# Kernel tuning notes

Hardware: AMD Instinct MI355X
Metric: run time of the kernel (lower is better)

## Reference

```python
import jax, jax.numpy as jnp
import numpy as np

N, D_IN, D_ATTN = 8192, 48, 8


def setup_inputs() -> dict:
    key = jax.random.key(0)
    ks = jax.random.split(key, 9)
    s = 1.0 / np.sqrt(D_IN)
    return {
        "x": jax.random.normal(ks[0], (N, D_IN), jnp.float32),
        "Kw": jax.random.normal(ks[1], (D_IN, D_ATTN), jnp.float32) * s,
        "Kb": jax.random.normal(ks[2], (D_ATTN,), jnp.float32) * s,
        "Qw": jax.random.normal(ks[3], (D_IN, D_ATTN), jnp.float32) * s,
        "Qb": jax.random.normal(ks[4], (D_ATTN,), jnp.float32) * s,
        "Vw": jax.random.normal(ks[5], (D_IN, D_ATTN), jnp.float32) * s,
        "Vb": jax.random.normal(ks[6], (D_ATTN,), jnp.float32) * s,
        "Zw": jax.random.normal(ks[7], (D_ATTN, D_IN), jnp.float32) * (1.0 / np.sqrt(D_ATTN)),
        "Zb": jax.random.normal(ks[8], (D_IN,), jnp.float32) * (1.0 / np.sqrt(D_ATTN)),
    }


def reference(x, Kw, Kb, Qw, Qb, Vw, Vb, Zw, Zb):
    # Tiny QKV projections: [N,48] -> [N,8]
    Xk = x @ Kw + Kb
    Xq = x @ Qw + Qb
    Xv = x @ Vw + Vb
    # Attention over the batch/row dimension: [N,8]@[8,N] -> [N,N]
    scale = jnp.sqrt(jnp.asarray(D_ATTN, jnp.float32))
    AM = jax.nn.softmax(Xk @ Xq.T / scale, axis=1)  # torch F.softmax 2D default dim=1
    Z = AM @ Xv                                      # [N,8]
    return x + (Z @ Zw + Zb)                         # residual + output proj [N,48]
```

## Files before the change

### kernel.cpp

```cpp
#include <hip/hip_runtime.h>


#define PART_OFF 98560

typedef _Float16 f16x2 __attribute__((ext_vector_type(2)));

union HU { unsigned u; f16x2 h; };

static __device__ __forceinline__ unsigned pku(float a, float b) {
    auto v = __builtin_amdgcn_cvt_pkrtz(a, b);
    union { decltype(v) v2; unsigned u; } t;
    t.v2 = v;
    return t.u;
}
static __device__ __forceinline__ f16x2 asH2(unsigned u) {
    HU t; t.u = u; return t.h;
}
static __device__ __forceinline__ float fdot2(f16x2 a, f16x2 b, float c) {
#if __has_builtin(__builtin_amdgcn_fdot2)
    return __builtin_amdgcn_fdot2(a, b, c, false);
#else
    return fmaf((float)a.x, (float)b.x, fmaf((float)a.y, (float)b.y, c));
#endif
}

__global__ __launch_bounds__(256) void proj_kernel(
    const float* __restrict__ x,
    const float* __restrict__ Kw, const float* __restrict__ Kb,
    const float* __restrict__ Qw, const float* __restrict__ Qb,
    const float* __restrict__ Vw, const float* __restrict__ Vb,
    unsigned* __restrict__ Xksf16, unsigned* __restrict__ Qf16,
    unsigned* __restrict__ Vf16, unsigned int* __restrict__ qmax2_bits)
{
    __shared__ float xs[32 * 49];
    __shared__ float wAll[3 * 388];
    __shared__ float bs[24];
    __shared__ float outv[32][25];
    const int tid = threadIdx.x;
    const int r0 = blockIdx.x * 32;

    for (int i = tid; i < 1536; i += 256) {
        int r = i / 48, c = i - r * 48;
        xs[r * 49 + c] = x[r0 * 48 + i];
    }
    for (int i = tid; i < 384; i += 256) {
        wAll[i]       = Kw[i];
        wAll[388 + i] = Qw[i];
        wAll[776 + i] = Vw[i];
    }
    if (tid < 8)       bs[tid] = Kb[tid];
    else if (tid < 16) bs[tid] = Qb[tid - 8];
    else if (tid < 24) bs[tid] = Vb[tid - 16];
    __syncthreads();

    const int rl = tid >> 3;
    const int g  = tid & 7;
    const int c0 = 3 * g;
    const float* xr = &xs[rl * 49];
    const float* w0 = &wAll[((c0 + 0) >> 3) * 388 + ((c0 + 0) & 7)];
    const float* w1 = &wAll[((c0 + 1) >> 3) * 388 + ((c0 + 1) & 7)];
    const float* w2 = &wAll[((c0 + 2) >> 3) * 388 + ((c0 + 2) & 7)];
    float a0 = bs[c0], a1 = bs[c0 + 1], a2 = bs[c0 + 2];
    #pragma unroll
    for (int k = 0; k < 48; k++) {
        const float xv = xr[k];
        a0 = fmaf(xv, w0[k * 8], a0);
        a1 = fmaf(xv, w1[k * 8], a1);
        a2 = fmaf(xv, w2[k * 8], a2);
    }
    outv[rl][c0] = a0; outv[rl][c0 + 1] = a1; outv[rl][c0 + 2] = a2;
    __syncthreads();

    const float kscale = 0.51008732149f;
    if (tid < 32) {
        uint4 o;
        o.x = pku(outv[tid][0] * kscale, outv[tid][1] * kscale);
        o.y = pku(outv[tid][2] * kscale, outv[tid][3] * kscale);
        o.z = pku(outv[tid][4] * kscale, outv[tid][5] * kscale);
        o.w = pku(outv[tid][6] * kscale, outv[tid][7] * kscale);
        ((uint4*)Xksf16)[r0 + tid] = o;
    } else if (tid < 64) {
        const int r = tid - 32;
        uint4 o;
        o.x = pku(outv[r][8],  outv[r][9]);
        o.y = pku(outv[r][10], outv[r][11]);
        o.z = pku(outv[r][12], outv[r][13]);
        o.w = pku(outv[r][14], outv[r][15]);
        ((uint4*)Qf16)[r0 + r] = o;
    } else if (tid < 192) {
        const int t2 = tid - 64;
        const int p = t2 >> 3, c = t2 & 7;
        Vf16[(blockIdx.x * 16 + p) * 8 + c] =
            pku(outv[2 * p][16 + c], outv[2 * p + 1][16 + c]);
    } else if (tid < 224) {
        const int r = tid - 192;
        float n2 = 0.f;
        #pragma unroll
        for (int c = 0; c < 8; c++) n2 = fmaf(outv[r][8 + c], outv[r][8 + c], n2);
        #pragma unroll
        for (int off = 16; off > 0; off >>= 1)
            n2 = fmaxf(n2, __shfl_xor(n2, off, 64));
        if (r == 0) atomicMax(qmax2_bits, __float_as_uint(n2));
    }
}

__global__ __launch_bounds__(256) void attn_kernel(
    const unsigned* __restrict__ Xksf16, const unsigned* __restrict__ Qf16,
    const unsigned* __restrict__ Vf16,
    const unsigned int* __restrict__ qmax2_bits,
    float* __restrict__ part)
{
    const int tid   = threadIdx.x;
    const int wave  = tid >> 6, lane = tid & 63;
    const int rg    = blockIdx.x & 255;
    const int chunk = blockIdx.x >> 8;
    const int rw0   = rg * 32 + wave * 8;

    const float qmax2 = __uint_as_float(*qmax2_bits);

    f16x2 k2[8][4];
    float sinit[8], l[8], acc[8][8];
    #pragma unroll
    for (int r = 0; r < 8; r++) {
        const uint4 kv = ((const uint4*)Xksf16)[rw0 + r];
        k2[r][0] = asH2(kv.x); k2[r][1] = asH2(kv.y);
        k2[r][2] = asH2(kv.z); k2[r][3] = asH2(kv.w);
        float kn2 = fdot2(k2[r][0], k2[r][0], 0.f);
        kn2 = fdot2(k2[r][1], k2[r][1], kn2);
        kn2 = fdot2(k2[r][2], k2[r][2], kn2);
        kn2 = fdot2(k2[r][3], k2[r][3], kn2);
        sinit[r] = -sqrtf(kn2 * qmax2);
        l[r] = 0.f;
        #pragma unroll
        for (int c = 0; c < 8; c++) acc[r][c] = 0.f;
    }

    const f16x2 one2 = asH2(pku(1.f, 1.f));
    const uint4* Q4 = (const uint4*)Qf16;
    const uint4* V4 = (const uint4*)Vf16;

    const int P0 = chunk * 512 + lane;
    #pragma unroll 2
    for (int s = 0; s < 8; s++) {
        const int p = P0 + s * 64;
        const uint4 qa = Q4[2 * p];
        const uint4 qb = Q4[2 * p + 1];
        const uint4 va = V4[2 * p];
        const uint4 vb = V4[2 * p + 1];
        f16x2 qa2[4] = {asH2(qa.x), asH2(qa.y), asH2(qa.z), asH2(qa.w)};
        f16x2 qb2[4] = {asH2(qb.x), asH2(qb.y), asH2(qb.z), asH2(qb.w)};
        f16x2 v2[8]  = {asH2(va.x), asH2(va.y), asH2(va.z), asH2(va.w),
                        asH2(vb.x), asH2(vb.y), asH2(vb.z), asH2(vb.w)};
        #pragma unroll
        for (int r = 0; r < 8; r++) {
            float s0 = fdot2(k2[r][0], qa2[0], sinit[r]);
            s0 = fdot2(k2[r][1], qa2[1], s0);
            s0 = fdot2(k2[r][2], qa2[2], s0);
            s0 = fdot2(k2[r][3], qa2[3], s0);
            float s1 = fdot2(k2[r][0], qb2[0], sinit[r]);
            s1 = fdot2(k2[r][1], qb2[1], s1);
            s1 = fdot2(k2[r][2], qb2[2], s1);
            s1 = fdot2(k2[r][3], qb2[3], s1);
            const f16x2 ph = asH2(pku(__builtin_amdgcn_exp2f(s0),
                                      __builtin_amdgcn_exp2f(s1)));
            l[r] = fdot2(ph, one2, l[r]);
            acc[r][0] = fdot2(ph, v2[0], acc[r][0]);
            acc[r][1] = fdot2(ph, v2[1], acc[r][1]);
            acc[r][2] = fdot2(ph, v2[2], acc[r][2]);
            acc[r][3] = fdot2(ph, v2[3], acc[r][3]);
            acc[r][4] = fdot2(ph, v2[4], acc[r][4]);
            acc[r][5] = fdot2(ph, v2[5], acc[r][5]);
            acc[r][6] = fdot2(ph, v2[6], acc[r][6]);
            acc[r][7] = fdot2(ph, v2[7], acc[r][7]);
        }
    }

    #pragma unroll
    for (int m = 1; m < 64; m <<= 1) {
        #pragma unroll
        for (int r = 0; r < 8; r++) {
            l[r] += __shfl_xor(l[r], m, 64);
            #pragma unroll
            for (int c = 0; c < 8; c++) acc[r][c] += __shfl_xor(acc[r][c], m, 64);
        }
    }
    if (lane == 0) {
        float* pr = part + ((size_t)chunk * 8192 + rw0) * 12;
        #pragma unroll
        for (int r = 0; r < 8; r++) {
            #pragma unroll
            for (int c = 0; c < 8; c++) pr[r * 12 + c] = acc[r][c];
            pr[r * 12 + 8] = l[r];
        }
    }
}

__global__ __launch_bounds__(256) void finish_kernel(
    const float* __restrict__ x,
    const float* __restrict__ Zw, const float* __restrict__ Zb,
    const float* __restrict__ part, float* __restrict__ out)
{
    __shared__ float Zs[128 * 9];
    __shared__ float zw_s[384];
    __shared__ float zb_s[48];
    const int tid = threadIdx.x;
    const int r0 = blockIdx.x * 128;

    for (int i = tid; i < 384; i += 256) zw_s[i] = Zw[i];
    if (tid < 48) zb_s[tid] = Zb[tid];

    if (tid < 128) {
        const int row = r0 + tid;
        float a[9];
        #pragma unroll
        for (int c = 0; c < 9; c++) a[c] = 0.f;
        #pragma unroll
        for (int ch = 0; ch < 8; ch++) {
            const float* p = part + ((size_t)ch * 8192 + row) * 12;
            #pragma unroll
            for (int c = 0; c < 9; c++) a[c] += p[c];
        }
        const float inv = 1.0f / a[8];
        #pragma unroll
        for (int c = 0; c < 8; c++) Zs[tid * 9 + c] = a[c] * inv;
    }
    __syncthreads();

    for (int e = tid; e < 128 * 48; e += 256) {
        const int r = e / 48, c = e - r * 48;
        float o = x[r0 * 48 + e] + zb_s[c];
        #pragma unroll
        for (int k = 0; k < 8; k++) o = fmaf(Zs[r * 9 + k], zw_s[k * 48 + c], o);
        out[r0 * 48 + e] = o;
    }
}

extern "C" void kernel_launch(void* const* d_in, const int* in_sizes, int n_in,
                              void* d_out, int out_size, void* d_ws, size_t ws_size,
                              hipStream_t stream) {
    const float* x  = (const float*)d_in[0];
    const float* Kw = (const float*)d_in[1];
    const float* Kb = (const float*)d_in[2];
    const float* Qw = (const float*)d_in[3];
    const float* Qb = (const float*)d_in[4];
    const float* Vw = (const float*)d_in[5];
    const float* Vb = (const float*)d_in[6];
    const float* Zw = (const float*)d_in[7];
    const float* Zb = (const float*)d_in[8];
    float* out = (float*)d_out;

    float* ws = (float*)d_ws;
    unsigned* Xksf16 = (unsigned*)ws;
    unsigned* Qf16   = (unsigned*)(ws + 32768);
    unsigned* Vf16   = (unsigned*)(ws + 65536);
    unsigned int* qmax2_bits = (unsigned int*)(ws + 98304);
    float* part = ws + PART_OFF;

    (void)hipMemsetAsync(qmax2_bits, 0, sizeof(unsigned int), stream);
    proj_kernel<<<256, 256, 0, stream>>>(x, Kw, Kb, Qw, Qb, Vw, Vb,
                                         Xksf16, Qf16, Vf16, qmax2_bits);
    attn_kernel<<<2048, 256, 0, stream>>>(Xksf16, Qf16, Vf16, qmax2_bits, part);
    finish_kernel<<<64, 256, 0, stream>>>(x, Zw, Zb, part, out);
}
```

Before: 131.6 us.

## Map one query row per lane and accumulate key chunks via atomics

The attention kernel now gives each lane its own row, so the 64-step cross-lane shuffle reduction goes away. All lanes walk the same 128-key chunk, so the Q/V loads are wave-uniform broadcasts, and Q and V are interleaved into one buffer. Partial sums from the 64 chunks are combined with float atomicAdd into a zeroed accumulator, which replaces the partials buffer and the finish-kernel reduction. In exchange it adds a memset, 9 atomics per row per chunk (64-way contention per address) and nondeterministic summation order.

```diff
diff --git a/kernel.cpp b/kernel.cpp
--- a/kernel.cpp
+++ b/kernel.cpp
@@ -1,7 +1,9 @@
 #include <hip/hip_runtime.h>
 
 
-#define PART_OFF 98560
+#define QV_OFF   32768
+#define QMAX_OFF 98304
+#define ACC_OFF  98560
 
 typedef _Float16 f16x2 __attribute__((ext_vector_type(2)));
 
@@ -29,8 +31,8 @@
     const float* __restrict__ Kw, const float* __restrict__ Kb,
     const float* __restrict__ Qw, const float* __restrict__ Qb,
     const float* __restrict__ Vw, const float* __restrict__ Vb,
-    unsigned* __restrict__ Xksf16, unsigned* __restrict__ Qf16,
-    unsigned* __restrict__ Vf16, unsigned int* __restrict__ qmax2_bits)
+    unsigned* __restrict__ Xksf16, unsigned* __restrict__ QV,
+    unsigned int* __restrict__ qmax2_bits)
 {
     __shared__ float xs[32 * 49];
     __shared__ float wAll[3 * 388];
@@ -81,17 +83,18 @@
         ((uint4*)Xksf16)[r0 + tid] = o;
     } else if (tid < 64) {
         const int r = tid - 32;
+        const int j = r0 + r;
         uint4 o;
         o.x = pku(outv[r][8],  outv[r][9]);
         o.y = pku(outv[r][10], outv[r][11]);
         o.z = pku(outv[r][12], outv[r][13]);
         o.w = pku(outv[r][14], outv[r][15]);
-        ((uint4*)Qf16)[r0 + r] = o;
+        ((uint4*)QV)[(j >> 1) * 4 + (j & 1)] = o;
     } else if (tid < 192) {
         const int t2 = tid - 64;
         const int p = t2 >> 3, c = t2 & 7;
-        Vf16[(blockIdx.x * 16 + p) * 8 + c] =
-            pku(outv[2 * p][16 + c], outv[2 * p + 1][16 + c]);
+        const int pg = blockIdx.x * 16 + p;
+        QV[pg * 16 + 8 + c] = pku(outv[2 * p][16 + c], outv[2 * p + 1][16 + c]);
     } else if (tid < 224) {
         const int r = tid - 192;
         float n2 = 0.f;
@@ -105,100 +108,70 @@
 }
 
 __global__ __launch_bounds__(256) void attn_kernel(
-    const unsigned* __restrict__ Xksf16, const unsigned* __restrict__ Qf16,
-    const unsigned* __restrict__ Vf16,
+    const unsigned* __restrict__ Xksf16, const unsigned* __restrict__ QV,
     const unsigned int* __restrict__ qmax2_bits,
-    float* __restrict__ part)
+    float* __restrict__ accG)
 {
     const int tid   = threadIdx.x;
     const int wave  = tid >> 6, lane = tid & 63;
-    const int rg    = blockIdx.x & 255;
-    const int chunk = blockIdx.x >> 8;
-    const int rw0   = rg * 32 + wave * 8;
+    const int rgrp  = blockIdx.x & 31;
+    const int chunk = blockIdx.x >> 5;
+    const int row   = rgrp * 256 + wave * 64 + lane;
 
     const float qmax2 = __uint_as_float(*qmax2_bits);
 
-    f16x2 k2[8][4];
-    float sinit[8], l[8], acc[8][8];
+    const uint4 kv = ((const uint4*)Xksf16)[row];
+    f16x2 k2[4] = {asH2(kv.x), asH2(kv.y), asH2(kv.z), asH2(kv.w)};
+    float kn2 = fdot2(k2[0], k2[0], 0.f);
+    kn2 = fdot2(k2[1], k2[1], kn2);
+    kn2 = fdot2(k2[2], k2[2], kn2);
+    kn2 = fdot2(k2[3], k2[3], kn2);
+    const float sinit = -sqrtf(kn2 * qmax2);
+
+    float l = 0.f, acc[8];
     #pragma unroll
-    for (int r = 0; r < 8; r++) {
-        const uint4 kv = ((const uint4*)Xksf16)[rw0 + r];
-        k2[r][0] = asH2(kv.x); k2[r][1] = asH2(kv.y);
-        k2[r][2] = asH2(kv.z); k2[r][3] = asH2(kv.w);
-        float kn2 = fdot2(k2[r][0], k2[r][0], 0.f);
-        kn2 = fdot2(k2[r][1], k2[r][1], kn2);
-        kn2 = fdot2(k2[r][2], k2[r][2], kn2);
-        kn2 = fdot2(k2[r][3], k2[r][3], kn2);
-        sinit[r] = -sqrtf(kn2 * qmax2);
-        l[r] = 0.f;
-        #pragma unroll
-        for (int c = 0; c < 8; c++) acc[r][c] = 0.f;
-    }
-
-    const f16x2 one2 = asH2(pku(1.f, 1.f));
-    const uint4* Q4 = (const uint4*)Qf16;
-    const uint4* V4 = (const uint4*)Vf16;
-
-    const int P0 = chunk * 512 + lane;
-    #pragma unroll 2
-    for (int s = 0; s < 8; s++) {
-        const int p = P0 + s * 64;
-        const uint4 qa = Q4[2 * p];
-        const uint4 qb = Q4[2 * p + 1];
-        const uint4 va = V4[2 * p];
-        const uint4 vb = V4[2 * p + 1];
-        f16x2 qa2[4] = {asH2(qa.x), asH2(qa.y), asH2(qa.z), asH2(qa.w)};
-        f16x2 qb2[4] = {asH2(qb.x), asH2(qb.y), asH2(qb.z), asH2(qb.w)};
-        f16x2 v2[8]  = {asH2(va.x), asH2(va.y), asH2(va.z), asH2(va.w),
-                        asH2(vb.x), asH2(vb.y), asH2(vb.z), asH2(vb.w)};
-        #pragma unroll
-        for (int r = 0; r < 8; r++) {
-            float s0 = fdot2(k2[r][0], qa2[0], sinit[r]);
-            s0 = fdot2(k2[r][1], qa2[1], s0);
-            s0 = fdot2(k2[r][2], qa2[2], s0);
-            s0 = fdot2(k2[r][3], qa2[3], s0);
-            float s1 = fdot2(k2[r][0], qb2[0], sinit[r]);
-            s1 = fdot2(k2[r][1], qb2[1], s1);
-            s1 = fdot2(k2[r][2], qb2[2], s1);
-            s1 = fdot2(k2[r][3], qb2[3], s1);
-            const f16x2 ph = asH2(pku(__builtin_amdgcn_exp2f(s0),
-                                      __builtin_amdgcn_exp2f(s1)));
-            l[r] = fdot2(ph, one2, l[r]);
-            acc[r][0] = fdot2(ph, v2[0], acc[r][0]);
-            acc[r][1] = fdot2(ph, v2[1], acc[r][1]);
-            acc[r][2] = fdot2(ph, v2[2], acc[r][2]);
-            acc[r][3] = fdot2(ph, v2[3], acc[r][3]);
-            acc[r][4] = fdot2(ph, v2[4], acc[r][4]);
-            acc[r][5] = fdot2(ph, v2[5], acc[r][5]);
-            acc[r][6] = fdot2(ph, v2[6], acc[r][6]);
-            acc[r][7] = fdot2(ph, v2[7], acc[r][7]);
-        }
-    }
-
+    for (int c = 0; c < 8; c++) acc[c] = 0.f;
+
+    const f16x2 one2 = asH2(0x3C003C00u);
+    const uint4* QV4 = (const uint4*)QV + (size_t)chunk * 64 * 4;
+
+    #pragma unroll 4
+    for (int p = 0; p < 64; p++) {
+        const uint4 qa = QV4[p * 4 + 0];
+        const uint4 qb = QV4[p * 4 + 1];
+        const uint4 va = QV4[p * 4 + 2];
+        const uint4 vb = QV4[p * 4 + 3];
+        float s0 = fdot2(k2[0], asH2(qa.x), sinit);
+        s0 = fdot2(k2[1], asH2(qa.y), s0);
+        s0 = fdot2(k2[2], asH2(qa.z), s0);
+        s0 = fdot2(k2[3], asH2(qa.w), s0);
+        float s1 = fdot2(k2[0], asH2(qb.x), sinit);
+        s1 = fdot2(k2[1], asH2(qb.y), s1);
+        s1 = fdot2(k2[2], asH2(qb.z), s1);
+        s1 = fdot2(k2[3], asH2(qb.w), s1);
+        const f16x2 ph = asH2(pku(__builtin_amdgcn_exp2f(s0),
+                                  __builtin_amdgcn_exp2f(s1)));
+        l = fdot2(ph, one2, l);
+        acc[0] = fdot2(ph, asH2(va.x), acc[0]);
+        acc[1] = fdot2(ph, asH2(va.y), acc[1]);
+        acc[2] = fdot2(ph, asH2(va.z), acc[2]);
+        acc[3] = fdot2(ph, asH2(va.w), acc[3]);
+        acc[4] = fdot2(ph, asH2(vb.x), acc[4]);
+        acc[5] = fdot2(ph, asH2(vb.y), acc[5]);
+        acc[6] = fdot2(ph, asH2(vb.z), acc[6]);
+        acc[7] = fdot2(ph, asH2(vb.w), acc[7]);
+    }
+
+    float* dst = accG + (size_t)row * 16;
     #pragma unroll
-    for (int m = 1; m < 64; m <<= 1) {
-        #pragma unroll
-        for (int r = 0; r < 8; r++) {
-            l[r] += __shfl_xor(l[r], m, 64);
-            #pragma unroll
-            for (int c = 0; c < 8; c++) acc[r][c] += __shfl_xor(acc[r][c], m, 64);
-        }
-    }
-    if (lane == 0) {
-        float* pr = part + ((size_t)chunk * 8192 + rw0) * 12;
-        #pragma unroll
-        for (int r = 0; r < 8; r++) {
-            #pragma unroll
-            for (int c = 0; c < 8; c++) pr[r * 12 + c] = acc[r][c];
-            pr[r * 12 + 8] = l[r];
-        }
-    }
+    for (int c = 0; c < 8; c++) atomicAdd(dst + c, acc[c]);
+    atomicAdd(dst + 8, l);
 }
 
 __global__ __launch_bounds__(256) void finish_kernel(
     const float* __restrict__ x,
     const float* __restrict__ Zw, const float* __restrict__ Zb,
-    const float* __restrict__ part, float* __restrict__ out)
+    const float* __restrict__ accG, float* __restrict__ out)
 {
     __shared__ float Zs[128 * 9];
     __shared__ float zw_s[384];
@@ -211,15 +184,7 @@
 
     if (tid < 128) {
         const int row = r0 + tid;
-        float a[9];
-        #pragma unroll
-        for (int c = 0; c < 9; c++) a[c] = 0.f;
-        #pragma unroll
-        for (int ch = 0; ch < 8; ch++) {
-            const float* p = part + ((size_t)ch * 8192 + row) * 12;
-            #pragma unroll
-            for (int c = 0; c < 9; c++) a[c] += p[c];
-        }
+        const float* a = accG + (size_t)row * 16;
         const float inv = 1.0f / a[8];
         #pragma unroll
         for (int c = 0; c < 8; c++) Zs[tid * 9 + c] = a[c] * inv;
@@ -251,14 +216,14 @@
 
     float* ws = (float*)d_ws;
     unsigned* Xksf16 = (unsigned*)ws;
-    unsigned* Qf16   = (unsigned*)(ws + 32768);
-    unsigned* Vf16   = (unsigned*)(ws + 65536);
-    unsigned int* qmax2_bits = (unsigned int*)(ws + 98304);
-    float* part = ws + PART_OFF;
+    unsigned* QV     = (unsigned*)(ws + QV_OFF);
+    unsigned int* qmax2_bits = (unsigned int*)(ws + QMAX_OFF);
+    float* accG = ws + ACC_OFF;
 
     (void)hipMemsetAsync(qmax2_bits, 0, sizeof(unsigned int), stream);
+    (void)hipMemsetAsync(accG, 0, 8192 * 16 * sizeof(float), stream);
     proj_kernel<<<256, 256, 0, stream>>>(x, Kw, Kb, Qw, Qb, Vw, Vb,
-                                         Xksf16, Qf16, Vf16, qmax2_bits);
-    attn_kernel<<<2048, 256, 0, stream>>>(Xksf16, Qf16, Vf16, qmax2_bits, part);
-    finish_kernel<<<64, 256, 0, stream>>>(x, Zw, Zb, part, out);
-}
+                                         Xksf16, QV, qmax2_bits);
+    attn_kernel<<<2048, 256, 0, stream>>>(Xksf16, QV, qmax2_bits, accG);
+    finish_kernel<<<64, 256, 0, stream>>>(x, Zw, Zb, accG, out);
+}
```

New measurement: 351.8 us. 2.67x slower.
